# Kernel tuning notes

Hardware: AMD Instinct MI355X
Metric: run time of the kernel (lower is better)

The kernel has to match this reference:

```python
import jax, jax.numpy as jnp
import numpy as np

D = 256
H1, H2 = 256, 128

def setup_inputs() -> dict:
    key0 = jax.random.key(0)
    ks = jax.random.split(key0, 10)
    B, Lq, Lk = 2, 512, 512
    query = jax.random.normal(ks[0], (B, Lq, D), dtype=jnp.float32)
    key_t = jax.random.normal(ks[1], (B, Lk, D), dtype=jnp.float32)
    value = jax.random.normal(ks[2], (B, Lk, D), dtype=jnp.float32)
    mask = jnp.ones((B, Lq, Lk), dtype=jnp.int32)
    s1 = 1.0 / np.sqrt(2 * D)
    W1 = jax.random.uniform(ks[3], (2 * D, H1), jnp.float32, -s1, s1)  # torch Linear(2D,H1), [in,out]
    b1 = jax.random.uniform(ks[4], (H1,), jnp.float32, -s1, s1)
    s2 = 1.0 / np.sqrt(H1)
    W2 = jax.random.uniform(ks[5], (H1, H2), jnp.float32, -s2, s2)
    b2 = jax.random.uniform(ks[6], (H2,), jnp.float32, -s2, s2)
    s3 = 1.0 / np.sqrt(H2)
    W3 = jax.random.uniform(ks[7], (H2, 1), jnp.float32, -s3, s3)
    b3 = jax.random.uniform(ks[8], (1,), jnp.float32, -s3, s3)
    return {"query": query, "key": key_t, "value": value, "mask": mask,
            "W1": W1, "b1": b1, "W2": W2, "b2": b2, "W3": W3, "b3": b3}

def reference(query, key, value, mask, W1, b1, W2, b2, W3, b3):
    # Original: cat([q_i, k_j]) @ W1 == q_i @ W1[:D] + k_j @ W1[D:]  (algebraic split,
    # identical math, avoids materializing the [B,Lq,Lk,2D] concat tensor).
    W1q, W1k = W1[:D], W1[D:]
    qp = jnp.einsum('bqd,dh->bqh', query, W1q)           # [B,Lq,H1]
    kp = jnp.einsum('bkd,dh->bkh', key, W1k)             # [B,Lk,H1]
    h1 = jax.nn.relu(qp[:, :, None, :] + kp[:, None, :, :] + b1)   # [B,Lq,Lk,H1]
    h2 = jax.nn.relu(jnp.einsum('bqkh,hj->bqkj', h1, W2) + b2)      # [B,Lq,Lk,H2]
    scores = (jnp.einsum('bqkj,jo->bqko', h2, W3) + b3)[..., 0]     # [B,Lq,Lk]
    scores = jnp.where(mask == 0, jnp.float32(-1e9), scores)
    attn = jax.nn.softmax(scores, axis=-1)               # dropout is identity in eval mode
    out = jnp.einsum('bqk,bkd->bqd', attn, value)
    return out, attn
```

## Files before the change

kernel.cpp:

```cpp
#include <hip/hip_runtime.h>

#define D_  256
#define H1_ 256
#define H2_ 128
#define B_  2
#define LQ_ 512
#define LK_ 512
#define BK  64

typedef float  f32x4  __attribute__((ext_vector_type(4)));
typedef __bf16 bf16x8 __attribute__((ext_vector_type(8)));
typedef __bf16 bf16x4 __attribute__((ext_vector_type(4)));

__global__ __launch_bounds__(512) void prep_kernel(
    const float* __restrict__ query, const float* __restrict__ key,
    const float* __restrict__ W1, const float* __restrict__ b1,
    const float* __restrict__ W2,
    float* __restrict__ qp, float* __restrict__ kp, __bf16* __restrict__ w2f) {
  const int blk = blockIdx.x;
  const int tid = threadIdx.x;
  if (blk >= 512) {
    const int id   = (blk - 512) * 512 + tid;
    const int j    = id & 7;
    const int lane = (id >> 3) & 63;
    const int frag = id >> 9;
    const int nt = frag & 3;
    const int wn = (frag >> 2) & 1;
    const int ks = (frag >> 3) & 1;
    const int kc = frag >> 4;
    const int n = wn * 64 + nt * 16 + (lane & 15);
    const int k = kc * 64 + ks * 32 + ((lane >> 4) << 3) + j;
    w2f[id] = (__bf16)W2[k * H2_ + n];
    return;
  }
  __shared__ float in_lds[4][D_];
  __shared__ float part[4][H1_];
  const int row0 = blk * 4;
  const int sel  = row0 >> 10;
  const float* __restrict__ src = sel ? key : query;
  const int base = (row0 & 1023) * D_;
  for (int i = tid; i < 4 * D_; i += 512)
    in_lds[i >> 8][i & 255] = src[base + i];
  __syncthreads();
  const int h  = tid & 255;
  const int kh = tid >> 8;
  float acc[4] = {0.f, 0.f, 0.f, 0.f};
  const float* __restrict__ w = W1 + sel * D_ * H1_ + kh * 128 * H1_ + h;
#pragma unroll 4
  for (int dd = 0; dd < 128; ++dd) {
    const float wv = w[dd * H1_];
    const int d = kh * 128 + dd;
#pragma unroll
    for (int r = 0; r < 4; ++r) acc[r] += in_lds[r][d] * wv;
  }
  if (kh == 1) {
#pragma unroll
    for (int r = 0; r < 4; ++r) part[r][h] = acc[r];
  }
  __syncthreads();
  if (kh == 0) {
    const float bias = sel ? 0.0f : b1[h];
    float* __restrict__ dst = sel ? kp : qp;
#pragma unroll
    for (int r = 0; r < 4; ++r)
      dst[base + r * H1_ + h] = acc[r] + part[r][h] + bias;
  }
}

__global__ __launch_bounds__(256, 2) void score_kernel(
    const float* __restrict__ qp, const float* __restrict__ kp,
    const __bf16* __restrict__ w2f,
    const float* __restrict__ b2, const float* __restrict__ W3,
    const float* __restrict__ b3, float* __restrict__ scores) {
  __shared__ __align__(16) __bf16 A_lds[128 * BK];
  __shared__ float  spart[2][128];

  const int b  = blockIdx.z;
  const int q0 = blockIdx.y * 8;
  const int k0 = blockIdx.x * 16;
  const int tid  = threadIdx.x;
  const int wave = tid >> 6;
  const int lane = tid & 63;
  const int quad = lane >> 4;
  const int l16  = lane & 15;
  const int wm   = wave >> 1;
  const int wn   = wave & 1;
  const int h8   = l16 & 7;

  const int qi = tid >> 5;
  const int t5 = (tid >> 4) & 1;
  const int kg = tid & 15;

  const float* __restrict__ qpb = qp + (b * LQ_ + q0) * H1_;
  const float* __restrict__ kpb = kp + (b * LK_ + k0) * H1_;

  f32x4 acc[4][4];
#pragma unroll
  for (int mt = 0; mt < 4; ++mt)
#pragma unroll
    for (int nt = 0; nt < 4; ++nt)
      acc[mt][nt] = (f32x4){0.f, 0.f, 0.f, 0.f};

  for (int kc = 0; kc < H1_ / BK; ++kc) {
    bf16x8 bfr[2][4];
#pragma unroll
    for (int ks = 0; ks < 2; ++ks)
#pragma unroll
      for (int nt = 0; nt < 4; ++nt)
        bfr[ks][nt] = *(const bf16x8*)(
            w2f + ((((kc * 2 + ks) * 2 + wn) * 4 + nt) * 64 + lane) * 8);

    const float4 qv = *(const float4*)(qpb + qi * H1_ + kc * BK + kg * 4);
#pragma unroll
    for (int ii = 0; ii < 8; ++ii) {
      const int ki = t5 * 8 + ii;
      const int r  = qi * 16 + ki;
      const float4 kv = *(const float4*)(kpb + ki * H1_ + kc * BK + kg * 4);
      bf16x4 a;
      a[0] = (__bf16)fmaxf(qv.x + kv.x, 0.f);
      a[1] = (__bf16)fmaxf(qv.y + kv.y, 0.f);
      a[2] = (__bf16)fmaxf(qv.z + kv.z, 0.f);
      a[3] = (__bf16)fmaxf(qv.w + kv.w, 0.f);
      const int sw = (((kg >> 1) ^ (r & 7)) << 3) + ((kg & 1) << 2);
      *(bf16x4*)(&A_lds[r * BK + sw]) = a;
    }
    __syncthreads();
#pragma unroll
    for (int ks = 0; ks < 2; ++ks) {
      const int cbase = ks * 4 + quad;
      bf16x8 af[4];
#pragma unroll
      for (int mt = 0; mt < 4; ++mt) {
        const int ra = wm * 64 + mt * 16 + l16;
        af[mt] = *(const bf16x8*)(&A_lds[ra * BK + ((cbase ^ h8) << 3)]);
      }
#pragma unroll
      for (int mt = 0; mt < 4; ++mt)
#pragma unroll
        for (int nt = 0; nt < 4; ++nt)
          acc[mt][nt] = __builtin_amdgcn_mfma_f32_16x16x32_bf16(
              af[mt], bfr[ks][nt], acc[mt][nt], 0, 0, 0);
    }
    __syncthreads();
  }

  float part[4][4];
#pragma unroll
  for (int mt = 0; mt < 4; ++mt)
#pragma unroll
    for (int rg = 0; rg < 4; ++rg) part[mt][rg] = 0.f;
#pragma unroll
  for (int nt = 0; nt < 4; ++nt) {
    const int col = wn * 64 + nt * 16 + l16;
    const float b2v = b2[col];
    const float w3v = W3[col];
#pragma unroll
    for (int mt = 0; mt < 4; ++mt)
#pragma unroll
      for (int rg = 0; rg < 4; ++rg) {
        float h2 = acc[mt][nt][rg] + b2v;
        h2 = fmaxf(h2, 0.f);
        part[mt][rg] += h2 * w3v;
      }
  }
#pragma unroll
  for (int off = 1; off < 16; off <<= 1)
#pragma unroll
    for (int mt = 0; mt < 4; ++mt)
#pragma unroll
      for (int rg = 0; rg < 4; ++rg)
        part[mt][rg] += __shfl_xor(part[mt][rg], off, 64);
  if (l16 == 0) {
#pragma unroll
    for (int mt = 0; mt < 4; ++mt)
#pragma unroll
      for (int rg = 0; rg < 4; ++rg) {
        const int rl = wm * 64 + mt * 16 + quad * 4 + rg;
        spart[wn][rl] = part[mt][rg];
      }
  }
  __syncthreads();
  if (tid < 128) {
    const float s = spart[0][tid] + spart[1][tid] + b3[0];
    const int qi2 = tid >> 4, ki2 = tid & 15;
    scores[(b * LQ_ + q0 + qi2) * LK_ + k0 + ki2] = s;
  }
}

__global__ __launch_bounds__(512) void smout_kernel(
    const float* __restrict__ sc, float* __restrict__ attn,
    const int* __restrict__ mask, const float* __restrict__ value,
    float* __restrict__ out) {
  const int qg = blockIdx.x, b = blockIdx.y;
  const int tid = threadIdx.x;
  __shared__ __align__(16) float a_lds[LK_][4];
  __shared__ __align__(16) f32x4 p_lds[7][4][64];
  const int row0 = b * LQ_ + qg * 4;
  const int w = tid >> 6, lane = tid & 63;
  if (w < 4) {
    const float* __restrict__ srow = sc + (row0 + w) * LK_;
    const int*  __restrict__ mrow = mask + (row0 + w) * LK_;
    float v[8];
#pragma unroll
    for (int j = 0; j < 8; ++j) {
      float s = srow[lane + j * 64];
      if (mrow[lane + j * 64] == 0) s = -1e9f;
      v[j] = s;
    }
    float m = v[0];
#pragma unroll
    for (int j = 1; j < 8; ++j) m = fmaxf(m, v[j]);
#pragma unroll
    for (int off = 32; off; off >>= 1) m = fmaxf(m, __shfl_xor(m, off, 64));
    float sum = 0.f;
#pragma unroll
    for (int j = 0; j < 8; ++j) { v[j] = __expf(v[j] - m); sum += v[j]; }
#pragma unroll
    for (int off = 32; off; off >>= 1) sum += __shfl_xor(sum, off, 64);
    const float inv = 1.f / sum;
    float* __restrict__ arow = attn + (row0 + w) * LK_;
#pragma unroll
    for (int j = 0; j < 8; ++j) {
      const float p = v[j] * inv;
      a_lds[lane + j * 64][w] = p;
      arow[lane + j * 64] = p;
    }
  }
  __syncthreads();
  const int kh2 = tid >> 6;
  const int dv  = tid & 63;
  f32x4 acc[4];
#pragma unroll
  for (int q = 0; q < 4; ++q) acc[q] = (f32x4){0.f, 0.f, 0.f, 0.f};
  const f32x4* __restrict__ vb4 = (const f32x4*)value + (b * LK_ + kh2 * 64) * 64 + dv;
#pragma unroll 4
  for (int k = 0; k < 64; ++k) {
    const f32x4 v4 = vb4[k * 64];
    const f32x4 p4 = *(const f32x4*)(&a_lds[kh2 * 64 + k][0]);
#pragma unroll
    for (int q = 0; q < 4; ++q) acc[q] += p4[q] * v4;
  }
  if (kh2 > 0) {
#pragma unroll
    for (int q = 0; q < 4; ++q) p_lds[kh2 - 1][q][dv] = acc[q];
  }
  __syncthreads();
  if (kh2 == 0) {
    f32x4* __restrict__ ob4 = (f32x4*)out + row0 * 64 + dv;
#pragma unroll
    for (int q = 0; q < 4; ++q) {
      f32x4 r = acc[q];
#pragma unroll
      for (int pp = 0; pp < 7; ++pp) r += p_lds[pp][q][dv];
      ob4[q * 64] = r;
    }
  }
}

extern "C" void kernel_launch(void* const* d_in, const int* in_sizes, int n_in,
                              void* d_out, int out_size, void* d_ws, size_t ws_size,
                              hipStream_t stream) {
  (void)in_sizes; (void)n_in; (void)out_size; (void)ws_size;
  const float* query = (const float*)d_in[0];
  const float* key   = (const float*)d_in[1];
  const float* value = (const float*)d_in[2];
  const int*   mask  = (const int*)d_in[3];
  const float* W1    = (const float*)d_in[4];
  const float* b1    = (const float*)d_in[5];
  const float* W2    = (const float*)d_in[6];
  const float* b2    = (const float*)d_in[7];
  const float* W3    = (const float*)d_in[8];
  const float* b3    = (const float*)d_in[9];

  float* out  = (float*)d_out;
  float* attn = out + B_ * LQ_ * D_;

  float*  qp  = (float*)d_ws;
  float*  kp  = qp + B_ * LQ_ * H1_;
  __bf16* w2f = (__bf16*)(kp + B_ * LK_ * H1_);
  float*  sc  = (float*)(w2f + H2_ * H1_);

  prep_kernel<<<576, 512, 0, stream>>>(query, key, W1, b1, W2, qp, kp, w2f);
  dim3 gscore(LK_ / 16, LQ_ / 8, B_);
  score_kernel<<<gscore, 256, 0, stream>>>(qp, kp, w2f, b2, W3, b3, sc);
  smout_kernel<<<dim3(128, B_), 512, 0, stream>>>(sc, attn, mask, value, out);
}
```

Baseline: 141.1 us.

## Double-buffer LDS tile and prefetch next chunk during MFMA in score kernel

The score kernel's H1 reduction loop now uses two LDS buffers for the relu(qp+kp) tile. It prefetches the next chunk's qp/kp values and W2 fragments into registers before issuing the current MFMAs, then writes the next tile into the alternate buffer afterward. This leaves one barrier per iteration instead of two and aims to hide global load latency behind matrix math. In exchange it doubles LDS use for the tile and raises register pressure, which at launch_bounds(256,2) could cause spills or lower occupancy.

```diff
diff --git a/kernel.cpp b/kernel.cpp
--- a/kernel.cpp
+++ b/kernel.cpp
@@ -72,7 +72,7 @@
     const __bf16* __restrict__ w2f,
     const float* __restrict__ b2, const float* __restrict__ W3,
     const float* __restrict__ b3, float* __restrict__ scores) {
-  __shared__ __align__(16) __bf16 A_lds[128 * BK];
+  __shared__ __align__(16) __bf16 A_lds[2][128 * BK];
   __shared__ float  spart[2][128];
 
   const int b  = blockIdx.z;
@@ -101,30 +101,51 @@
     for (int nt = 0; nt < 4; ++nt)
       acc[mt][nt] = (f32x4){0.f, 0.f, 0.f, 0.f};
 
-  for (int kc = 0; kc < H1_ / BK; ++kc) {
-    bf16x8 bfr[2][4];
-#pragma unroll
-    for (int ks = 0; ks < 2; ++ks)
-#pragma unroll
-      for (int nt = 0; nt < 4; ++nt)
-        bfr[ks][nt] = *(const bf16x8*)(
-            w2f + ((((kc * 2 + ks) * 2 + wn) * 4 + nt) * 64 + lane) * 8);
-
-    const float4 qv = *(const float4*)(qpb + qi * H1_ + kc * BK + kg * 4);
+  {
+    const float4 qv = *(const float4*)(qpb + qi * H1_ + kg * 4);
 #pragma unroll
     for (int ii = 0; ii < 8; ++ii) {
       const int ki = t5 * 8 + ii;
       const int r  = qi * 16 + ki;
-      const float4 kv = *(const float4*)(kpb + ki * H1_ + kc * BK + kg * 4);
+      const float4 kv = *(const float4*)(kpb + ki * H1_ + kg * 4);
       bf16x4 a;
       a[0] = (__bf16)fmaxf(qv.x + kv.x, 0.f);
       a[1] = (__bf16)fmaxf(qv.y + kv.y, 0.f);
       a[2] = (__bf16)fmaxf(qv.z + kv.z, 0.f);
       a[3] = (__bf16)fmaxf(qv.w + kv.w, 0.f);
       const int sw = (((kg >> 1) ^ (r & 7)) << 3) + ((kg & 1) << 2);
-      *(bf16x4*)(&A_lds[r * BK + sw]) = a;
-    }
-    __syncthreads();
+      *(bf16x4*)(&A_lds[0][r * BK + sw]) = a;
+    }
+  }
+  bf16x8 bcur[2][4];
+#pragma unroll
+  for (int ks = 0; ks < 2; ++ks)
+#pragma unroll
+    for (int nt = 0; nt < 4; ++nt)
+      bcur[ks][nt] = *(const bf16x8*)(
+          w2f + (((ks * 2 + wn) * 4 + nt) * 64 + lane) * 8);
+  __syncthreads();
+
+#pragma unroll
+  for (int kc = 0; kc < 4; ++kc) {
+    const int cur = kc & 1;
+    float4 qv_n;
+    float4 kv_n[8];
+    bf16x8 bnxt[2][4];
+    if (kc < 3) {
+      qv_n = *(const float4*)(qpb + qi * H1_ + (kc + 1) * BK + kg * 4);
+#pragma unroll
+      for (int ii = 0; ii < 8; ++ii) {
+        const int ki = t5 * 8 + ii;
+        kv_n[ii] = *(const float4*)(kpb + ki * H1_ + (kc + 1) * BK + kg * 4);
+      }
+#pragma unroll
+      for (int ks = 0; ks < 2; ++ks)
+#pragma unroll
+        for (int nt = 0; nt < 4; ++nt)
+          bnxt[ks][nt] = *(const bf16x8*)(
+              w2f + (((((kc + 1) * 2 + ks) * 2 + wn) * 4 + nt) * 64 + lane) * 8);
+    }
 #pragma unroll
     for (int ks = 0; ks < 2; ++ks) {
       const int cbase = ks * 4 + quad;
@@ -132,14 +153,33 @@
 #pragma unroll
       for (int mt = 0; mt < 4; ++mt) {
         const int ra = wm * 64 + mt * 16 + l16;
-        af[mt] = *(const bf16x8*)(&A_lds[ra * BK + ((cbase ^ h8) << 3)]);
+        af[mt] = *(const bf16x8*)(&A_lds[cur][ra * BK + ((cbase ^ h8) << 3)]);
       }
 #pragma unroll
       for (int mt = 0; mt < 4; ++mt)
 #pragma unroll
         for (int nt = 0; nt < 4; ++nt)
           acc[mt][nt] = __builtin_amdgcn_mfma_f32_16x16x32_bf16(
-              af[mt], bfr[ks][nt], acc[mt][nt], 0, 0, 0);
+              af[mt], bcur[ks][nt], acc[mt][nt], 0, 0, 0);
+    }
+    if (kc < 3) {
+#pragma unroll
+      for (int ii = 0; ii < 8; ++ii) {
+        const int ki = t5 * 8 + ii;
+        const int r  = qi * 16 + ki;
+        bf16x4 a;
+        a[0] = (__bf16)fmaxf(qv_n.x + kv_n[ii].x, 0.f);
+        a[1] = (__bf16)fmaxf(qv_n.y + kv_n[ii].y, 0.f);
+        a[2] = (__bf16)fmaxf(qv_n.z + kv_n[ii].z, 0.f);
+        a[3] = (__bf16)fmaxf(qv_n.w + kv_n[ii].w, 0.f);
+        const int sw = (((kg >> 1) ^ (r & 7)) << 3) + ((kg & 1) << 2);
+        *(bf16x4*)(&A_lds[cur ^ 1][r * BK + sw]) = a;
+      }
+#pragma unroll
+      for (int ks = 0; ks < 2; ++ks)
+#pragma unroll
+        for (int nt = 0; nt < 4; ++nt)
+          bcur[ks][nt] = bnxt[ks][nt];
     }
     __syncthreads();
   }
```

Result: slower. 147.5 us (+4.5%).
